# Kernel tuning notes

Measured on AMD Instinct MI355X. Metric: run time of the kernel, lower is better.

The kernel has to match this reference:

```python
import jax, jax.numpy as jnp
import numpy as np

N = 50000
E = 800000
IN_DIM = 128
HIDDEN = 96
HEADS = 4
HEAD_DIM = HIDDEN // HEADS
NUM_LAYERS = 3
NEG_SLOPE = 0.2


def _gat_layer(h, W, a_l, a_r, b, src, dst):
    # h: [N, F_in], W: [F_in, H*D], a_l/a_r: [H, D], b: [H, D]
    feat = (h @ W).reshape(N, HEADS, HEAD_DIM)          # [N, H, D]
    el = jnp.sum(feat * a_l, axis=-1)                    # [N, H]
    er = jnp.sum(feat * a_r, axis=-1)                    # [N, H]
    e = el[src] + er[dst]                                # [E, H]
    e = jnp.where(e > 0, e, NEG_SLOPE * e)               # leaky_relu
    # edge softmax over incoming edges of each dst node
    m = jax.ops.segment_max(e, dst, num_segments=N)      # [N, H]
    ex = jnp.exp(e - m[dst])                             # [E, H]
    denom = jax.ops.segment_sum(ex, dst, num_segments=N) # [N, H]
    alpha = ex / denom[dst]                              # [E, H]
    msg = feat[src] * alpha[:, :, None]                  # [E, H, D]
    out = jax.ops.segment_sum(msg, dst, num_segments=N)  # [N, H, D]
    out = out + b                                        # bias
    out = jax.nn.elu(out)                                # activation
    return out.reshape(N, HEADS * HEAD_DIM)              # flatten(1)


def setup_inputs() -> dict:
    key = jax.random.key(0)
    ks = jax.random.split(key, 16)
    feats = jax.random.normal(ks[0], (N, IN_DIM), dtype=jnp.float32)
    src = jax.random.randint(ks[1], (E,), 0, N)
    dst = jax.random.randint(ks[2], (E,), 0, N)
    inp = {"feats": feats, "src": src, "dst": dst}
    fin = IN_DIM
    for l in range(NUM_LAYERS):
        s = 1.0 / np.sqrt(fin)
        inp[f"W{l}"] = jax.random.normal(ks[3 + 4 * l], (fin, HIDDEN), dtype=jnp.float32) * s
        inp[f"al{l}"] = jax.random.normal(ks[4 + 4 * l], (HEADS, HEAD_DIM), dtype=jnp.float32) * 0.1
        inp[f"ar{l}"] = jax.random.normal(ks[5 + 4 * l], (HEADS, HEAD_DIM), dtype=jnp.float32) * 0.1
        inp[f"b{l}"] = jnp.zeros((HEADS, HEAD_DIM), dtype=jnp.float32)
        fin = HIDDEN
    return inp


def reference(feats, src, dst, W0, al0, ar0, b0, W1, al1, ar1, b1, W2, al2, ar2, b2):
    h = feats
    params = [(W0, al0, ar0, b0), (W1, al1, ar1, b1), (W2, al2, ar2, b2)]
    for (W, al, ar, b) in params:
        h = _gat_layer(h, W, al, ar, b, src, dst)
    # AvgPooling over all nodes (single graph) -> [1, HIDDEN]
    return jnp.mean(h, axis=0, keepdims=True)
```

## Files before the change

### kernel.cpp

```cpp
#include <hip/hip_runtime.h>
#include <hip/hip_bf16.h>

#define N_NODES 50000
#define E_EDGES 800000
#define IN_DIM  128
#define HIDDEN  96
#define HEADS   4
#define HEAD_DIM 24
#define NEG_SLOPE 0.2f
#define POOL_BLOCKS 256


__global__ void k_hist(const int* __restrict__ dst, int* __restrict__ deg) {
    int e = blockIdx.x * 256 + threadIdx.x;
    if (e < E_EDGES) atomicAdd(&deg[dst[e]], 1);
}

__global__ __launch_bounds__(256) void k_scan1(const int* __restrict__ deg,
                                               int* __restrict__ bsum, int n) {
    int i = blockIdx.x * 256 + threadIdx.x;
    int v = (i < n) ? deg[i] : 0;
#pragma unroll
    for (int s = 1; s < 64; s <<= 1) v += __shfl_xor(v, s);
    __shared__ int ws[4];
    if ((threadIdx.x & 63) == 0) ws[threadIdx.x >> 6] = v;
    __syncthreads();
    if (threadIdx.x == 0) bsum[blockIdx.x] = ws[0] + ws[1] + ws[2] + ws[3];
}

__global__ __launch_bounds__(256) void k_scan3(const int* __restrict__ deg,
                                               const int* __restrict__ bsum,
                                               int* __restrict__ off, int n) {
    int tid = threadIdx.x;
    int lane = tid & 63, wv = tid >> 6;

    int pv = (tid < blockIdx.x) ? bsum[tid] : 0;
#pragma unroll
    for (int s = 1; s < 64; s <<= 1) pv += __shfl_xor(pv, s);

    int i = blockIdx.x * 256 + tid;
    int v = (i < n) ? deg[i] : 0;
    int x = v;
#pragma unroll
    for (int s = 1; s < 64; s <<= 1) {
        int t = __shfl_up(x, s);
        if (lane >= s) x += t;
    }

    __shared__ int wsum[4], wsum2[4];
    if (lane == 63) wsum[wv] = x;
    if (lane == 0)  wsum2[wv] = pv;
    __syncthreads();
    int add = wsum2[0] + wsum2[1] + wsum2[2] + wsum2[3];
    for (int w = 0; w < wv; ++w) add += wsum[w];
    if (i < n) off[i] = x - v + add;
    if (i == n - 1) off[n] = x + add;
}

__global__ void k_fill(const int* __restrict__ src, const int* __restrict__ dst,
                       const int* __restrict__ off, int* __restrict__ cursor,
                       int* __restrict__ ssrc) {
    int e = blockIdx.x * 256 + threadIdx.x;
    if (e < E_EDGES) {
        int d = dst[e];
        int p = off[d] + atomicAdd(&cursor[d], 1);
        ssrc[p] = src[e];
    }
}


template <int K>
__global__ __launch_bounds__(384) void k_gemm(const float* __restrict__ h,
                                              const float* __restrict__ W,
                                              const float* __restrict__ al_g,
                                              const float* __restrict__ ar_g,
                                              float* __restrict__ feat,
                                              float* __restrict__ el,
                                              float* __restrict__ er, int n) {
    constexpr int HL = 64 * K;
    constexpr int PT = 384 * 17;
    constexpr int SM = (HL > PT) ? HL : PT;
    __shared__ float smem[SM];
    float* hl = smem;

    int node0 = blockIdx.x * 64;
    int total4 = 64 * K / 4;
    for (int idx = threadIdx.x; idx < total4; idx += 384) {
        int node = idx / (K / 4);
        int koff = (idx % (K / 4)) * 4;
        float4 v = make_float4(0.f, 0.f, 0.f, 0.f);
        if (node0 + node < n)
            v = *(const float4*)(&h[(size_t)(node0 + node) * K + koff]);
        *(float4*)(&hl[node * K + koff]) = v;
    }
    __syncthreads();
    int grp = threadIdx.x / 48;
    int c = (threadIdx.x % 48) * 2;
    int nb = grp * 8;
    float acc[8][2];
#pragma unroll
    for (int i = 0; i < 8; ++i) acc[i][0] = acc[i][1] = 0.f;
    for (int k = 0; k < K; k += 4) {
        float2 w0 = *(const float2*)&W[(k + 0) * 96 + c];
        float2 w1 = *(const float2*)&W[(k + 1) * 96 + c];
        float2 w2 = *(const float2*)&W[(k + 2) * 96 + c];
        float2 w3 = *(const float2*)&W[(k + 3) * 96 + c];
#pragma unroll
        for (int i = 0; i < 8; ++i) {
            float4 hv = *(const float4*)&hl[(nb + i) * K + k];
            acc[i][0] = fmaf(hv.x, w0.x, acc[i][0]);
            acc[i][1] = fmaf(hv.x, w0.y, acc[i][1]);
            acc[i][0] = fmaf(hv.y, w1.x, acc[i][0]);
            acc[i][1] = fmaf(hv.y, w1.y, acc[i][1]);
            acc[i][0] = fmaf(hv.z, w2.x, acc[i][0]);
            acc[i][1] = fmaf(hv.z, w2.y, acc[i][1]);
            acc[i][0] = fmaf(hv.w, w3.x, acc[i][0]);
            acc[i][1] = fmaf(hv.w, w3.y, acc[i][1]);
        }
    }
#pragma unroll
    for (int i = 0; i < 8; ++i) {
        int node = node0 + nb + i;
        if (node < n) *(float2*)&feat[(size_t)node * 96 + c] = make_float2(acc[i][0], acc[i][1]);
    }
    float alc0 = al_g[c], alc1 = al_g[c + 1];
    float arc0 = ar_g[c], arc1 = ar_g[c + 1];
    __syncthreads();
    float* part = smem;
    int base = threadIdx.x * 17;
#pragma unroll
    for (int i = 0; i < 8; ++i) {
        part[base + i * 2]     = acc[i][0] * alc0 + acc[i][1] * alc1;
        part[base + i * 2 + 1] = acc[i][0] * arc0 + acc[i][1] * arc1;
    }
    __syncthreads();
    if (threadIdx.x < 256) {
        int ig = threadIdx.x >> 2;
        int hh = threadIdx.x & 3;
        int g2 = ig >> 3, il = ig & 7;
        float se = 0.f, sr = 0.f;
#pragma unroll
        for (int cc = 0; cc < 12; ++cc) {
            int t = g2 * 48 + hh * 12 + cc;
            se += part[t * 17 + il * 2];
            sr += part[t * 17 + il * 2 + 1];
        }
        int node = node0 + ig;
        if (node < n) {
            el[node * 4 + hh] = se;
            er[node * 4 + hh] = sr;
        }
    }
}

__global__ __launch_bounds__(256) void k_agg(const int* __restrict__ off,
                                             const int* __restrict__ ssrc,
                                             const float* __restrict__ el,
                                             const float* __restrict__ er,
                                             const float* __restrict__ feat,
                                             const float* __restrict__ bias,
                                             float* __restrict__ out) {
    int n = blockIdx.x * 4 + (threadIdx.x >> 6);
    if (n >= N_NODES) return;
    int lane = threadIdx.x & 63;
    int j0   = lane >> 3;
    int h    = (lane >> 1) & 3;
    int half = lane & 1;
    int cbase = h * 24 + half * 12;
    unsigned cboff = (unsigned)cbase * 4u;

    int start = off[n], deg = off[n + 1] - start;
    float er_h = er[(unsigned)n * 4u + h];

    float e_reg[4];
    unsigned s_reg[4];
    float lmax = -1e30f;
#pragma unroll
    for (int t = 0; t < 4; ++t) {
        int j = t * 8 + j0;
        bool act = (j < deg);
        unsigned s = act ? (unsigned)ssrc[start + j] : 0u;
        float e = -1e30f;
        if (act) {
            e = el[s * 4u + h] + er_h;
            e = (e > 0.f) ? e : NEG_SLOPE * e;
        }
        s_reg[t] = s;
        e_reg[t] = e;
        lmax = fmaxf(lmax, e);
    }
    for (int j = 32 + j0; j < deg; j += 8) {
        unsigned s = (unsigned)ssrc[start + j];
        float e = el[s * 4u + h] + er_h;
        e = (e > 0.f) ? e : NEG_SLOPE * e;
        lmax = fmaxf(lmax, e);
    }
    lmax = fmaxf(lmax, __shfl_xor(lmax, 8));
    lmax = fmaxf(lmax, __shfl_xor(lmax, 16));
    lmax = fmaxf(lmax, __shfl_xor(lmax, 32));
    float m = lmax;

    float acc[12];
#pragma unroll
    for (int c = 0; c < 12; ++c) acc[c] = 0.f;
    float den = 0.f;
#pragma unroll
    for (int t = 0; t < 4; ++t) {
        int j = t * 8 + j0;
        if (j < deg) {
            float ex = __expf(e_reg[t] - m);
            den += ex;
            const float* fr = (const float*)((const char*)feat + (size_t)(s_reg[t] * 384u + cboff));
            float4 v0 = *(const float4*)(fr + 0);
            float4 v1 = *(const float4*)(fr + 4);
            float4 v2 = *(const float4*)(fr + 8);
            acc[0] = fmaf(ex, v0.x, acc[0]);  acc[1] = fmaf(ex, v0.y, acc[1]);
            acc[2] = fmaf(ex, v0.z, acc[2]);  acc[3] = fmaf(ex, v0.w, acc[3]);
            acc[4] = fmaf(ex, v1.x, acc[4]);  acc[5] = fmaf(ex, v1.y, acc[5]);
            acc[6] = fmaf(ex, v1.z, acc[6]);  acc[7] = fmaf(ex, v1.w, acc[7]);
            acc[8] = fmaf(ex, v2.x, acc[8]);  acc[9] = fmaf(ex, v2.y, acc[9]);
            acc[10] = fmaf(ex, v2.z, acc[10]); acc[11] = fmaf(ex, v2.w, acc[11]);
        }
    }
    for (int j = 32 + j0; j < deg; j += 8) {
        unsigned s = (unsigned)ssrc[start + j];
        float e = el[s * 4u + h] + er_h;
        e = (e > 0.f) ? e : NEG_SLOPE * e;
        float ex = __expf(e - m);
        den += ex;
        const float* fr = (const float*)((const char*)feat + (size_t)(s * 384u + cboff));
        float4 v0 = *(const float4*)(fr + 0);
        float4 v1 = *(const float4*)(fr + 4);
        float4 v2 = *(const float4*)(fr + 8);
        acc[0] = fmaf(ex, v0.x, acc[0]);  acc[1] = fmaf(ex, v0.y, acc[1]);
        acc[2] = fmaf(ex, v0.z, acc[2]);  acc[3] = fmaf(ex, v0.w, acc[3]);
        acc[4] = fmaf(ex, v1.x, acc[4]);  acc[5] = fmaf(ex, v1.y, acc[5]);
        acc[6] = fmaf(ex, v1.z, acc[6]);  acc[7] = fmaf(ex, v1.w, acc[7]);
        acc[8] = fmaf(ex, v2.x, acc[8]);  acc[9] = fmaf(ex, v2.y, acc[9]);
        acc[10] = fmaf(ex, v2.z, acc[10]); acc[11] = fmaf(ex, v2.w, acc[11]);
    }

#pragma unroll
    for (int st = 8; st <= 32; st <<= 1) {
        den += __shfl_xor(den, st);
#pragma unroll
        for (int c = 0; c < 12; ++c) acc[c] += __shfl_xor(acc[c], st);
    }

    if (j0 == 0) {
        float rden = (den > 0.f) ? 1.f / den : 0.f;
        const float* bp = &bias[cbase];
        float o[12];
#pragma unroll
        for (int c = 0; c < 12; ++c) {
            float v = acc[c] * rden + bp[c];
            o[c] = (v > 0.f) ? v : (__expf(v) - 1.f);
        }
        float* op = &out[(size_t)n * 96 + cbase];
        *(float4*)(op + 0) = make_float4(o[0], o[1], o[2], o[3]);
        *(float4*)(op + 4) = make_float4(o[4], o[5], o[6], o[7]);
        *(float4*)(op + 8) = make_float4(o[8], o[9], o[10], o[11]);
    }
}

__global__ __launch_bounds__(384) void k_pool1(const float* __restrict__ h,
                                               float* __restrict__ partial) {
    int r = threadIdx.x / 96;
    int c = threadIdx.x % 96;
    float a = 0.f;
    for (int nrow = blockIdx.x * 4 + r; nrow < N_NODES; nrow += POOL_BLOCKS * 4)
        a += h[(size_t)nrow * 96 + c];
    __shared__ float sred[4][96];
    sred[r][c] = a;
    __syncthreads();
    if (r == 0)
        partial[blockIdx.x * 96 + c] = sred[0][c] + sred[1][c] + sred[2][c] + sred[3][c];
}

__global__ __launch_bounds__(384) void k_pool2(const float* __restrict__ partial,
                                               float* __restrict__ out) {
    int g = threadIdx.x / 96;
    int c = threadIdx.x % 96;
    float a = 0.f;
    for (int b = g; b < POOL_BLOCKS; b += 4)
        a += partial[b * 96 + c];
    __shared__ float sred[4][96];
    sred[g][c] = a;
    __syncthreads();
    if (g == 0)
        out[c] = (sred[0][c] + sred[1][c] + sred[2][c] + sred[3][c]) * (1.0f / N_NODES);
}


extern "C" void kernel_launch(void* const* d_in, const int* in_sizes, int n_in,
                              void* d_out, int out_size, void* d_ws, size_t ws_size,
                              hipStream_t stream) {
    const float* feats = (const float*)d_in[0];
    const int* src = (const int*)d_in[1];
    const int* dst = (const int*)d_in[2];

    char* p = (char*)d_ws;
    auto alloc = [&](size_t bytes) {
        void* r = (void*)p;
        p += (bytes + 255) & ~(size_t)255;
        return r;
    };
    float* A       = (float*)alloc((size_t)N_NODES * 96 * 4);
    float* B       = (float*)alloc((size_t)N_NODES * 96 * 4);
    float* el      = (float*)alloc((size_t)N_NODES * 4 * 4);
    float* er      = (float*)alloc((size_t)N_NODES * 4 * 4);
    int* degcur    = (int*)alloc((size_t)N_NODES * 2 * 4);
    int* off       = (int*)alloc((size_t)(N_NODES + 1) * 4);
    int* bsum      = (int*)alloc((size_t)256 * 4);
    int* ssrc      = (int*)alloc((size_t)E_EDGES * 4);
    float* partial = (float*)alloc((size_t)POOL_BLOCKS * 96 * 4);
    int* deg = degcur;
    int* cursor = degcur + N_NODES;

    hipMemsetAsync(degcur, 0, (size_t)N_NODES * 2 * 4, stream);

    const int NB = (N_NODES + 255) / 256;
    k_hist<<<(E_EDGES + 255) / 256, 256, 0, stream>>>(dst, deg);
    k_scan1<<<NB, 256, 0, stream>>>(deg, bsum, N_NODES);
    k_scan3<<<NB, 256, 0, stream>>>(deg, bsum, off, N_NODES);
    k_fill<<<(E_EDGES + 255) / 256, 256, 0, stream>>>(src, dst, off, cursor, ssrc);

    const float* hin = feats;
    for (int l = 0; l < 3; ++l) {
        const float* W  = (const float*)d_in[3 + 4 * l];
        const float* al = (const float*)d_in[4 + 4 * l];
        const float* ar = (const float*)d_in[5 + 4 * l];
        const float* bb = (const float*)d_in[6 + 4 * l];

        if (l == 0)
            k_gemm<IN_DIM><<<(N_NODES + 63) / 64, 384, 0, stream>>>(hin, W, al, ar, B, el, er, N_NODES);
        else
            k_gemm<HIDDEN><<<(N_NODES + 63) / 64, 384, 0, stream>>>(hin, W, al, ar, B, el, er, N_NODES);

        k_agg<<<(N_NODES + 3) / 4, 256, 0, stream>>>(off, ssrc, el, er, B, bb, A);
        hin = A;
    }

    k_pool1<<<POOL_BLOCKS, 384, 0, stream>>>(A, partial);
    k_pool2<<<1, 384, 0, stream>>>(partial, (float*)d_out);
}
```

Before: 439.5 us.

## Fuse all GAT stages into one persistent cooperative kernel with grid syncs

Replaces the sequence of separate kernel launches (histogram, scans, fill, three GEMM/aggregate pairs, pooling) with one cooperative persistent kernel that loops over work with grid-stride tiles and uses grid.sync between phases. Layer-0 GEMM now runs before the CSR build inside the same launch. The aim is to remove launch overhead and the memset. The cost is that blocks are limited to the occupancy-resident count, and the aggregate phase uses 384-thread blocks with a large static shared array, which may lower occupancy. Each grid-wide barrier also adds latency.

```diff
diff --git a/kernel.cpp b/kernel.cpp
--- a/kernel.cpp
+++ b/kernel.cpp
@@ -1,303 +1,347 @@
 #include <hip/hip_runtime.h>
-#include <hip/hip_bf16.h>
+#include <hip/hip_cooperative_groups.h>
+
+namespace cg = cooperative_groups;
 
 #define N_NODES 50000
 #define E_EDGES 800000
 #define IN_DIM  128
 #define HIDDEN  96
-#define HEADS   4
-#define HEAD_DIM 24
 #define NEG_SLOPE 0.2f
-#define POOL_BLOCKS 256
-
-
-__global__ void k_hist(const int* __restrict__ dst, int* __restrict__ deg) {
-    int e = blockIdx.x * 256 + threadIdx.x;
-    if (e < E_EDGES) atomicAdd(&deg[dst[e]], 1);
-}
-
-__global__ __launch_bounds__(256) void k_scan1(const int* __restrict__ deg,
-                                               int* __restrict__ bsum, int n) {
-    int i = blockIdx.x * 256 + threadIdx.x;
-    int v = (i < n) ? deg[i] : 0;
-#pragma unroll
-    for (int s = 1; s < 64; s <<= 1) v += __shfl_xor(v, s);
-    __shared__ int ws[4];
-    if ((threadIdx.x & 63) == 0) ws[threadIdx.x >> 6] = v;
-    __syncthreads();
-    if (threadIdx.x == 0) bsum[blockIdx.x] = ws[0] + ws[1] + ws[2] + ws[3];
-}
-
-__global__ __launch_bounds__(256) void k_scan3(const int* __restrict__ deg,
-                                               const int* __restrict__ bsum,
-                                               int* __restrict__ off, int n) {
-    int tid = threadIdx.x;
-    int lane = tid & 63, wv = tid >> 6;
-
-    int pv = (tid < blockIdx.x) ? bsum[tid] : 0;
-#pragma unroll
-    for (int s = 1; s < 64; s <<= 1) pv += __shfl_xor(pv, s);
-
-    int i = blockIdx.x * 256 + tid;
-    int v = (i < n) ? deg[i] : 0;
-    int x = v;
-#pragma unroll
-    for (int s = 1; s < 64; s <<= 1) {
-        int t = __shfl_up(x, s);
-        if (lane >= s) x += t;
-    }
-
-    __shared__ int wsum[4], wsum2[4];
-    if (lane == 63) wsum[wv] = x;
-    if (lane == 0)  wsum2[wv] = pv;
-    __syncthreads();
-    int add = wsum2[0] + wsum2[1] + wsum2[2] + wsum2[3];
-    for (int w = 0; w < wv; ++w) add += wsum[w];
-    if (i < n) off[i] = x - v + add;
-    if (i == n - 1) off[n] = x + add;
-}
-
-__global__ void k_fill(const int* __restrict__ src, const int* __restrict__ dst,
-                       const int* __restrict__ off, int* __restrict__ cursor,
-                       int* __restrict__ ssrc) {
-    int e = blockIdx.x * 256 + threadIdx.x;
-    if (e < E_EDGES) {
-        int d = dst[e];
-        int p = off[d] + atomicAdd(&cursor[d], 1);
-        ssrc[p] = src[e];
-    }
-}
-
+#define NCH ((N_NODES + 255) / 256)
+
+struct Params {
+    const float* feats; const int* src; const int* dst;
+    const float* W[3]; const float* al[3]; const float* ar[3]; const float* bb[3];
+    float* A; float* B; float* el; float* er;
+    int* degcur; int* off; int* bsum; int* ssrc;
+    float* partial; float* out; int nblk;
+};
 
 template <int K>
-__global__ __launch_bounds__(384) void k_gemm(const float* __restrict__ h,
-                                              const float* __restrict__ W,
-                                              const float* __restrict__ al_g,
-                                              const float* __restrict__ ar_g,
-                                              float* __restrict__ feat,
-                                              float* __restrict__ el,
-                                              float* __restrict__ er, int n) {
-    constexpr int HL = 64 * K;
-    constexpr int PT = 384 * 17;
-    constexpr int SM = (HL > PT) ? HL : PT;
-    __shared__ float smem[SM];
-    float* hl = smem;
-
-    int node0 = blockIdx.x * 64;
-    int total4 = 64 * K / 4;
-    for (int idx = threadIdx.x; idx < total4; idx += 384) {
-        int node = idx / (K / 4);
-        int koff = (idx % (K / 4)) * 4;
-        float4 v = make_float4(0.f, 0.f, 0.f, 0.f);
-        if (node0 + node < n)
-            v = *(const float4*)(&h[(size_t)(node0 + node) * K + koff]);
-        *(float4*)(&hl[node * K + koff]) = v;
-    }
-    __syncthreads();
-    int grp = threadIdx.x / 48;
-    int c = (threadIdx.x % 48) * 2;
-    int nb = grp * 8;
-    float acc[8][2];
-#pragma unroll
-    for (int i = 0; i < 8; ++i) acc[i][0] = acc[i][1] = 0.f;
-    for (int k = 0; k < K; k += 4) {
-        float2 w0 = *(const float2*)&W[(k + 0) * 96 + c];
-        float2 w1 = *(const float2*)&W[(k + 1) * 96 + c];
-        float2 w2 = *(const float2*)&W[(k + 2) * 96 + c];
-        float2 w3 = *(const float2*)&W[(k + 3) * 96 + c];
+__device__ __forceinline__ void gemm_phase(const float* __restrict__ h,
+                                           const float* __restrict__ W,
+                                           const float* __restrict__ al_g,
+                                           const float* __restrict__ ar_g,
+                                           float* __restrict__ feat,
+                                           float* __restrict__ el,
+                                           float* __restrict__ er,
+                                           float* smem, int bid, int nblk) {
+    const int tid = threadIdx.x;
+    for (int t = bid; t * 64 < N_NODES; t += nblk) {
+        int node0 = t * 64;
+        int total4 = 64 * K / 4;
+        for (int idx = tid; idx < total4; idx += 384) {
+            int node = idx / (K / 4);
+            int koff = (idx % (K / 4)) * 4;
+            float4 v = make_float4(0.f, 0.f, 0.f, 0.f);
+            if (node0 + node < N_NODES)
+                v = *(const float4*)(&h[(size_t)(node0 + node) * K + koff]);
+            *(float4*)(&smem[node * K + koff]) = v;
+        }
+        __syncthreads();
+        int grp = tid / 48;
+        int c = (tid % 48) * 2;
+        int nb = grp * 8;
+        float acc[8][2];
+#pragma unroll
+        for (int i = 0; i < 8; ++i) acc[i][0] = acc[i][1] = 0.f;
+        for (int k = 0; k < K; k += 4) {
+            float2 w0 = *(const float2*)&W[(k + 0) * 96 + c];
+            float2 w1 = *(const float2*)&W[(k + 1) * 96 + c];
+            float2 w2 = *(const float2*)&W[(k + 2) * 96 + c];
+            float2 w3 = *(const float2*)&W[(k + 3) * 96 + c];
+#pragma unroll
+            for (int i = 0; i < 8; ++i) {
+                float4 hv = *(const float4*)&smem[(nb + i) * K + k];
+                acc[i][0] = fmaf(hv.x, w0.x, acc[i][0]);
+                acc[i][1] = fmaf(hv.x, w0.y, acc[i][1]);
+                acc[i][0] = fmaf(hv.y, w1.x, acc[i][0]);
+                acc[i][1] = fmaf(hv.y, w1.y, acc[i][1]);
+                acc[i][0] = fmaf(hv.z, w2.x, acc[i][0]);
+                acc[i][1] = fmaf(hv.z, w2.y, acc[i][1]);
+                acc[i][0] = fmaf(hv.w, w3.x, acc[i][0]);
+                acc[i][1] = fmaf(hv.w, w3.y, acc[i][1]);
+            }
+        }
 #pragma unroll
         for (int i = 0; i < 8; ++i) {
-            float4 hv = *(const float4*)&hl[(nb + i) * K + k];
-            acc[i][0] = fmaf(hv.x, w0.x, acc[i][0]);
-            acc[i][1] = fmaf(hv.x, w0.y, acc[i][1]);
-            acc[i][0] = fmaf(hv.y, w1.x, acc[i][0]);
-            acc[i][1] = fmaf(hv.y, w1.y, acc[i][1]);
-            acc[i][0] = fmaf(hv.z, w2.x, acc[i][0]);
-            acc[i][1] = fmaf(hv.z, w2.y, acc[i][1]);
-            acc[i][0] = fmaf(hv.w, w3.x, acc[i][0]);
-            acc[i][1] = fmaf(hv.w, w3.y, acc[i][1]);
-        }
-    }
-#pragma unroll
-    for (int i = 0; i < 8; ++i) {
-        int node = node0 + nb + i;
-        if (node < n) *(float2*)&feat[(size_t)node * 96 + c] = make_float2(acc[i][0], acc[i][1]);
-    }
-    float alc0 = al_g[c], alc1 = al_g[c + 1];
-    float arc0 = ar_g[c], arc1 = ar_g[c + 1];
-    __syncthreads();
-    float* part = smem;
-    int base = threadIdx.x * 17;
-#pragma unroll
-    for (int i = 0; i < 8; ++i) {
-        part[base + i * 2]     = acc[i][0] * alc0 + acc[i][1] * alc1;
-        part[base + i * 2 + 1] = acc[i][0] * arc0 + acc[i][1] * arc1;
-    }
-    __syncthreads();
-    if (threadIdx.x < 256) {
-        int ig = threadIdx.x >> 2;
-        int hh = threadIdx.x & 3;
-        int g2 = ig >> 3, il = ig & 7;
-        float se = 0.f, sr = 0.f;
-#pragma unroll
-        for (int cc = 0; cc < 12; ++cc) {
-            int t = g2 * 48 + hh * 12 + cc;
-            se += part[t * 17 + il * 2];
-            sr += part[t * 17 + il * 2 + 1];
-        }
-        int node = node0 + ig;
-        if (node < n) {
-            el[node * 4 + hh] = se;
-            er[node * 4 + hh] = sr;
-        }
-    }
-}
-
-__global__ __launch_bounds__(256) void k_agg(const int* __restrict__ off,
-                                             const int* __restrict__ ssrc,
-                                             const float* __restrict__ el,
-                                             const float* __restrict__ er,
-                                             const float* __restrict__ feat,
-                                             const float* __restrict__ bias,
-                                             float* __restrict__ out) {
-    int n = blockIdx.x * 4 + (threadIdx.x >> 6);
-    if (n >= N_NODES) return;
-    int lane = threadIdx.x & 63;
-    int j0   = lane >> 3;
-    int h    = (lane >> 1) & 3;
-    int half = lane & 1;
-    int cbase = h * 24 + half * 12;
-    unsigned cboff = (unsigned)cbase * 4u;
-
-    int start = off[n], deg = off[n + 1] - start;
-    float er_h = er[(unsigned)n * 4u + h];
-
-    float e_reg[4];
-    unsigned s_reg[4];
-    float lmax = -1e30f;
-#pragma unroll
-    for (int t = 0; t < 4; ++t) {
-        int j = t * 8 + j0;
-        bool act = (j < deg);
-        unsigned s = act ? (unsigned)ssrc[start + j] : 0u;
-        float e = -1e30f;
-        if (act) {
-            e = el[s * 4u + h] + er_h;
-            e = (e > 0.f) ? e : NEG_SLOPE * e;
-        }
-        s_reg[t] = s;
-        e_reg[t] = e;
-        lmax = fmaxf(lmax, e);
-    }
-    for (int j = 32 + j0; j < deg; j += 8) {
-        unsigned s = (unsigned)ssrc[start + j];
-        float e = el[s * 4u + h] + er_h;
-        e = (e > 0.f) ? e : NEG_SLOPE * e;
-        lmax = fmaxf(lmax, e);
-    }
-    lmax = fmaxf(lmax, __shfl_xor(lmax, 8));
-    lmax = fmaxf(lmax, __shfl_xor(lmax, 16));
-    lmax = fmaxf(lmax, __shfl_xor(lmax, 32));
-    float m = lmax;
-
-    float acc[12];
-#pragma unroll
-    for (int c = 0; c < 12; ++c) acc[c] = 0.f;
-    float den = 0.f;
-#pragma unroll
-    for (int t = 0; t < 4; ++t) {
-        int j = t * 8 + j0;
-        if (j < deg) {
-            float ex = __expf(e_reg[t] - m);
-            den += ex;
-            const float* fr = (const float*)((const char*)feat + (size_t)(s_reg[t] * 384u + cboff));
-            float4 v0 = *(const float4*)(fr + 0);
-            float4 v1 = *(const float4*)(fr + 4);
-            float4 v2 = *(const float4*)(fr + 8);
-            acc[0] = fmaf(ex, v0.x, acc[0]);  acc[1] = fmaf(ex, v0.y, acc[1]);
-            acc[2] = fmaf(ex, v0.z, acc[2]);  acc[3] = fmaf(ex, v0.w, acc[3]);
-            acc[4] = fmaf(ex, v1.x, acc[4]);  acc[5] = fmaf(ex, v1.y, acc[5]);
-            acc[6] = fmaf(ex, v1.z, acc[6]);  acc[7] = fmaf(ex, v1.w, acc[7]);
-            acc[8] = fmaf(ex, v2.x, acc[8]);  acc[9] = fmaf(ex, v2.y, acc[9]);
-            acc[10] = fmaf(ex, v2.z, acc[10]); acc[11] = fmaf(ex, v2.w, acc[11]);
-        }
-    }
-    for (int j = 32 + j0; j < deg; j += 8) {
-        unsigned s = (unsigned)ssrc[start + j];
-        float e = el[s * 4u + h] + er_h;
-        e = (e > 0.f) ? e : NEG_SLOPE * e;
-        float ex = __expf(e - m);
-        den += ex;
-        const float* fr = (const float*)((const char*)feat + (size_t)(s * 384u + cboff));
-        float4 v0 = *(const float4*)(fr + 0);
-        float4 v1 = *(const float4*)(fr + 4);
-        float4 v2 = *(const float4*)(fr + 8);
-        acc[0] = fmaf(ex, v0.x, acc[0]);  acc[1] = fmaf(ex, v0.y, acc[1]);
-        acc[2] = fmaf(ex, v0.z, acc[2]);  acc[3] = fmaf(ex, v0.w, acc[3]);
-        acc[4] = fmaf(ex, v1.x, acc[4]);  acc[5] = fmaf(ex, v1.y, acc[5]);
-        acc[6] = fmaf(ex, v1.z, acc[6]);  acc[7] = fmaf(ex, v1.w, acc[7]);
-        acc[8] = fmaf(ex, v2.x, acc[8]);  acc[9] = fmaf(ex, v2.y, acc[9]);
-        acc[10] = fmaf(ex, v2.z, acc[10]); acc[11] = fmaf(ex, v2.w, acc[11]);
-    }
-
-#pragma unroll
-    for (int st = 8; st <= 32; st <<= 1) {
-        den += __shfl_xor(den, st);
-#pragma unroll
-        for (int c = 0; c < 12; ++c) acc[c] += __shfl_xor(acc[c], st);
-    }
-
-    if (j0 == 0) {
-        float rden = (den > 0.f) ? 1.f / den : 0.f;
-        const float* bp = &bias[cbase];
-        float o[12];
-#pragma unroll
-        for (int c = 0; c < 12; ++c) {
-            float v = acc[c] * rden + bp[c];
-            o[c] = (v > 0.f) ? v : (__expf(v) - 1.f);
-        }
-        float* op = &out[(size_t)n * 96 + cbase];
-        *(float4*)(op + 0) = make_float4(o[0], o[1], o[2], o[3]);
-        *(float4*)(op + 4) = make_float4(o[4], o[5], o[6], o[7]);
-        *(float4*)(op + 8) = make_float4(o[8], o[9], o[10], o[11]);
-    }
-}
-
-__global__ __launch_bounds__(384) void k_pool1(const float* __restrict__ h,
-                                               float* __restrict__ partial) {
-    int r = threadIdx.x / 96;
-    int c = threadIdx.x % 96;
-    float a = 0.f;
-    for (int nrow = blockIdx.x * 4 + r; nrow < N_NODES; nrow += POOL_BLOCKS * 4)
-        a += h[(size_t)nrow * 96 + c];
-    __shared__ float sred[4][96];
-    sred[r][c] = a;
-    __syncthreads();
-    if (r == 0)
-        partial[blockIdx.x * 96 + c] = sred[0][c] + sred[1][c] + sred[2][c] + sred[3][c];
-}
-
-__global__ __launch_bounds__(384) void k_pool2(const float* __restrict__ partial,
-                                               float* __restrict__ out) {
-    int g = threadIdx.x / 96;
-    int c = threadIdx.x % 96;
-    float a = 0.f;
-    for (int b = g; b < POOL_BLOCKS; b += 4)
-        a += partial[b * 96 + c];
-    __shared__ float sred[4][96];
-    sred[g][c] = a;
-    __syncthreads();
-    if (g == 0)
-        out[c] = (sred[0][c] + sred[1][c] + sred[2][c] + sred[3][c]) * (1.0f / N_NODES);
+            int node = node0 + nb + i;
+            if (node < N_NODES)
+                *(float2*)&feat[(size_t)node * 96 + c] = make_float2(acc[i][0], acc[i][1]);
+        }
+        float alc0 = al_g[c], alc1 = al_g[c + 1];
+        float arc0 = ar_g[c], arc1 = ar_g[c + 1];
+        __syncthreads();
+        int base = tid * 17;
+#pragma unroll
+        for (int i = 0; i < 8; ++i) {
+            smem[base + i * 2]     = acc[i][0] * alc0 + acc[i][1] * alc1;
+            smem[base + i * 2 + 1] = acc[i][0] * arc0 + acc[i][1] * arc1;
+        }
+        __syncthreads();
+        if (tid < 256) {
+            int ig = tid >> 2;
+            int hh = tid & 3;
+            int g2 = ig >> 3, il = ig & 7;
+            float se = 0.f, sr = 0.f;
+#pragma unroll
+            for (int cc = 0; cc < 12; ++cc) {
+                int tt = g2 * 48 + hh * 12 + cc;
+                se += smem[tt * 17 + il * 2];
+                sr += smem[tt * 17 + il * 2 + 1];
+            }
+            int node = node0 + ig;
+            if (node < N_NODES) {
+                el[node * 4 + hh] = se;
+                er[node * 4 + hh] = sr;
+            }
+        }
+        __syncthreads();
+    }
+}
+
+__device__ __forceinline__ void agg_phase(const int* __restrict__ off,
+                                          const int* __restrict__ ssrc,
+                                          const float* __restrict__ el,
+                                          const float* __restrict__ er,
+                                          const float* __restrict__ feat,
+                                          const float* __restrict__ bias,
+                                          float* __restrict__ out, int bid, int nblk) {
+    const int tid = threadIdx.x;
+    const int lane = tid & 63;
+    const int wv = tid >> 6;
+    const int j0 = lane >> 3;
+    const int h = (lane >> 1) & 3;
+    const int half = lane & 1;
+    const int cbase = h * 24 + half * 12;
+    const unsigned cboff = (unsigned)cbase * 4u;
+
+    for (int base = bid * 6; base < N_NODES; base += nblk * 6) {
+        int n = base + wv;
+        if (n < N_NODES) {
+            int start = off[n], deg = off[n + 1] - start;
+            float er_h = er[(unsigned)n * 4u + h];
+
+            float e_reg[4];
+            unsigned s_reg[4];
+            float lmax = -1e30f;
+#pragma unroll
+            for (int t = 0; t < 4; ++t) {
+                int j = t * 8 + j0;
+                bool act = (j < deg);
+                unsigned s = act ? (unsigned)ssrc[start + j] : 0u;
+                float e = -1e30f;
+                if (act) {
+                    e = el[s * 4u + h] + er_h;
+                    e = (e > 0.f) ? e : NEG_SLOPE * e;
+                }
+                s_reg[t] = s;
+                e_reg[t] = e;
+                lmax = fmaxf(lmax, e);
+            }
+            for (int j = 32 + j0; j < deg; j += 8) {
+                unsigned s = (unsigned)ssrc[start + j];
+                float e = el[s * 4u + h] + er_h;
+                e = (e > 0.f) ? e : NEG_SLOPE * e;
+                lmax = fmaxf(lmax, e);
+            }
+            lmax = fmaxf(lmax, __shfl_xor(lmax, 8));
+            lmax = fmaxf(lmax, __shfl_xor(lmax, 16));
+            lmax = fmaxf(lmax, __shfl_xor(lmax, 32));
+            float m = lmax;
+
+            float acc[12];
+#pragma unroll
+            for (int c = 0; c < 12; ++c) acc[c] = 0.f;
+            float den = 0.f;
+#pragma unroll
+            for (int t = 0; t < 4; ++t) {
+                int j = t * 8 + j0;
+                if (j < deg) {
+                    float ex = __expf(e_reg[t] - m);
+                    den += ex;
+                    const float* fr = (const float*)((const char*)feat + (size_t)(s_reg[t] * 384u + cboff));
+                    float4 v0 = *(const float4*)(fr + 0);
+                    float4 v1 = *(const float4*)(fr + 4);
+                    float4 v2 = *(const float4*)(fr + 8);
+                    acc[0] = fmaf(ex, v0.x, acc[0]);   acc[1] = fmaf(ex, v0.y, acc[1]);
+                    acc[2] = fmaf(ex, v0.z, acc[2]);   acc[3] = fmaf(ex, v0.w, acc[3]);
+                    acc[4] = fmaf(ex, v1.x, acc[4]);   acc[5] = fmaf(ex, v1.y, acc[5]);
+                    acc[6] = fmaf(ex, v1.z, acc[6]);   acc[7] = fmaf(ex, v1.w, acc[7]);
+                    acc[8] = fmaf(ex, v2.x, acc[8]);   acc[9] = fmaf(ex, v2.y, acc[9]);
+                    acc[10] = fmaf(ex, v2.z, acc[10]); acc[11] = fmaf(ex, v2.w, acc[11]);
+                }
+            }
+            for (int j = 32 + j0; j < deg; j += 8) {
+                unsigned s = (unsigned)ssrc[start + j];
+                float e = el[s * 4u + h] + er_h;
+                e = (e > 0.f) ? e : NEG_SLOPE * e;
+                float ex = __expf(e - m);
+                den += ex;
+                const float* fr = (const float*)((const char*)feat + (size_t)(s * 384u + cboff));
+                float4 v0 = *(const float4*)(fr + 0);
+                float4 v1 = *(const float4*)(fr + 4);
+                float4 v2 = *(const float4*)(fr + 8);
+                acc[0] = fmaf(ex, v0.x, acc[0]);   acc[1] = fmaf(ex, v0.y, acc[1]);
+                acc[2] = fmaf(ex, v0.z, acc[2]);   acc[3] = fmaf(ex, v0.w, acc[3]);
+                acc[4] = fmaf(ex, v1.x, acc[4]);   acc[5] = fmaf(ex, v1.y, acc[5]);
+                acc[6] = fmaf(ex, v1.z, acc[6]);   acc[7] = fmaf(ex, v1.w, acc[7]);
+                acc[8] = fmaf(ex, v2.x, acc[8]);   acc[9] = fmaf(ex, v2.y, acc[9]);
+                acc[10] = fmaf(ex, v2.z, acc[10]); acc[11] = fmaf(ex, v2.w, acc[11]);
+            }
+
+#pragma unroll
+            for (int st = 8; st <= 32; st <<= 1) {
+                den += __shfl_xor(den, st);
+#pragma unroll
+                for (int c = 0; c < 12; ++c) acc[c] += __shfl_xor(acc[c], st);
+            }
+
+            if (j0 == 0) {
+                float rden = (den > 0.f) ? 1.f / den : 0.f;
+                const float* bp = &bias[cbase];
+                float o[12];
+#pragma unroll
+                for (int c = 0; c < 12; ++c) {
+                    float v = acc[c] * rden + bp[c];
+                    o[c] = (v > 0.f) ? v : (__expf(v) - 1.f);
+                }
+                float* op = &out[(size_t)n * 96 + cbase];
+                *(float4*)(op + 0) = make_float4(o[0], o[1], o[2], o[3]);
+                *(float4*)(op + 4) = make_float4(o[4], o[5], o[6], o[7]);
+                *(float4*)(op + 8) = make_float4(o[8], o[9], o[10], o[11]);
+            }
+        }
+    }
+}
+
+__device__ __forceinline__ void scan1_phase(const int* deg, int* bsum, int* ismem,
+                                            int bid, int nblk) {
+    const int tid = threadIdx.x;
+    for (int b = bid; b < NCH; b += nblk) {
+        int i = b * 256 + tid;
+        int v = (tid < 256 && i < N_NODES) ? deg[i] : 0;
+#pragma unroll
+        for (int s = 1; s < 64; s <<= 1) v += __shfl_xor(v, s);
+        if ((tid & 63) == 0) ismem[tid >> 6] = v;
+        __syncthreads();
+        if (tid == 0)
+            bsum[b] = ismem[0] + ismem[1] + ismem[2] + ismem[3] + ismem[4] + ismem[5];
+        __syncthreads();
+    }
+}
+
+__device__ __forceinline__ void scan3_phase(const int* deg, const int* bsum,
+                                            int* off, int* ismem, int bid, int nblk) {
+    const int tid = threadIdx.x;
+    const int lane = tid & 63, wv = tid >> 6;
+    for (int b = bid; b < NCH; b += nblk) {
+        int pv = (tid < b) ? bsum[tid] : 0;
+#pragma unroll
+        for (int s = 1; s < 64; s <<= 1) pv += __shfl_xor(pv, s);
+        int i = b * 256 + tid;
+        int v = (tid < 256 && i < N_NODES) ? deg[i] : 0;
+        int x = v;
+#pragma unroll
+        for (int s = 1; s < 64; s <<= 1) {
+            int t2 = __shfl_up(x, s);
+            if (lane >= s) x += t2;
+        }
+        if (lane == 63) ismem[wv] = x;
+        if (lane == 0)  ismem[8 + wv] = pv;
+        __syncthreads();
+        int add = ismem[8] + ismem[9] + ismem[10] + ismem[11] + ismem[12] + ismem[13];
+        for (int w = 0; w < wv; ++w) add += ismem[w];
+        if (tid < 256 && i < N_NODES) off[i] = x - v + add;
+        if (i == N_NODES - 1) off[N_NODES] = x + add;
+        __syncthreads();
+    }
+}
+
+__global__ __launch_bounds__(384) void mega(Params P) {
+    __shared__ float smem[8192];
+    int* ismem = (int*)smem;
+    cg::grid_group grid = cg::this_grid();
+    const int bid = blockIdx.x;
+    const int nblk = P.nblk;
+    const int tid = threadIdx.x;
+
+    for (int i = bid * 384 + tid; i < N_NODES * 2; i += nblk * 384) P.degcur[i] = 0;
+    gemm_phase<IN_DIM>(P.feats, P.W[0], P.al[0], P.ar[0], P.B, P.el, P.er, smem, bid, nblk);
+    grid.sync();
+
+    for (int e = bid * 384 + tid; e < E_EDGES; e += nblk * 384)
+        atomicAdd(&P.degcur[P.dst[e]], 1);
+    grid.sync();
+
+    scan1_phase(P.degcur, P.bsum, ismem, bid, nblk);
+    grid.sync();
+
+    scan3_phase(P.degcur, P.bsum, P.off, ismem, bid, nblk);
+    grid.sync();
+
+    {
+        int* cursor = P.degcur + N_NODES;
+        for (int e = bid * 384 + tid; e < E_EDGES; e += nblk * 384) {
+            int d = P.dst[e];
+            int p = P.off[d] + atomicAdd(&cursor[d], 1);
+            P.ssrc[p] = P.src[e];
+        }
+    }
+    grid.sync();
+
+    agg_phase(P.off, P.ssrc, P.el, P.er, P.B, P.bb[0], P.A, bid, nblk);
+    grid.sync();
+    gemm_phase<HIDDEN>(P.A, P.W[1], P.al[1], P.ar[1], P.B, P.el, P.er, smem, bid, nblk);
+    grid.sync();
+    agg_phase(P.off, P.ssrc, P.el, P.er, P.B, P.bb[1], P.A, bid, nblk);
+    grid.sync();
+    gemm_phase<HIDDEN>(P.A, P.W[2], P.al[2], P.ar[2], P.B, P.el, P.er, smem, bid, nblk);
+    grid.sync();
+    agg_phase(P.off, P.ssrc, P.el, P.er, P.B, P.bb[2], P.A, bid, nblk);
+    grid.sync();
+
+    {
+        int r = tid / 96, c = tid % 96;
+        float a = 0.f;
+        for (int nr = bid * 4 + r; nr < N_NODES; nr += nblk * 4)
+            a += P.A[(size_t)nr * 96 + c];
+        __syncthreads();
+        smem[tid] = a;
+        __syncthreads();
+        if (tid < 96)
+            P.partial[bid * 96 + tid] =
+                smem[tid] + smem[96 + tid] + smem[192 + tid] + smem[288 + tid];
+    }
+    grid.sync();
+
+    if (bid == 0) {
+        int g = tid / 96, c = tid % 96;
+        float a = 0.f;
+        for (int b = g; b < nblk; b += 4) a += P.partial[b * 96 + c];
+        smem[tid] = a;
+        __syncthreads();
+        if (tid < 96)
+            P.out[tid] = (smem[tid] + smem[96 + tid] + smem[192 + tid] + smem[288 + tid]) *
+                         (1.0f / N_NODES);
+    }
 }
 
 
 extern "C" void kernel_launch(void* const* d_in, const int* in_sizes, int n_in,
                               void* d_out, int out_size, void* d_ws, size_t ws_size,
                               hipStream_t stream) {
-    const float* feats = (const float*)d_in[0];
-    const int* src = (const int*)d_in[1];
-    const int* dst = (const int*)d_in[2];
+    Params pr;
+    pr.feats = (const float*)d_in[0];
+    pr.src   = (const int*)d_in[1];
+    pr.dst   = (const int*)d_in[2];
+    for (int l = 0; l < 3; ++l) {
+        pr.W[l]  = (const float*)d_in[3 + 4 * l];
+        pr.al[l] = (const float*)d_in[4 + 4 * l];
+        pr.ar[l] = (const float*)d_in[5 + 4 * l];
+        pr.bb[l] = (const float*)d_in[6 + 4 * l];
+    }
 
     char* p = (char*)d_ws;
     auto alloc = [&](size_t bytes) {
@@ -305,42 +349,29 @@
         p += (bytes + 255) & ~(size_t)255;
         return r;
     };
-    float* A       = (float*)alloc((size_t)N_NODES * 96 * 4);
-    float* B       = (float*)alloc((size_t)N_NODES * 96 * 4);
-    float* el      = (float*)alloc((size_t)N_NODES * 4 * 4);
-    float* er      = (float*)alloc((size_t)N_NODES * 4 * 4);
-    int* degcur    = (int*)alloc((size_t)N_NODES * 2 * 4);
-    int* off       = (int*)alloc((size_t)(N_NODES + 1) * 4);
-    int* bsum      = (int*)alloc((size_t)256 * 4);
-    int* ssrc      = (int*)alloc((size_t)E_EDGES * 4);
-    float* partial = (float*)alloc((size_t)POOL_BLOCKS * 96 * 4);
-    int* deg = degcur;
-    int* cursor = degcur + N_NODES;
-
-    hipMemsetAsync(degcur, 0, (size_t)N_NODES * 2 * 4, stream);
-
-    const int NB = (N_NODES + 255) / 256;
-    k_hist<<<(E_EDGES + 255) / 256, 256, 0, stream>>>(dst, deg);
-    k_scan1<<<NB, 256, 0, stream>>>(deg, bsum, N_NODES);
-    k_scan3<<<NB, 256, 0, stream>>>(deg, bsum, off, N_NODES);
-    k_fill<<<(E_EDGES + 255) / 256, 256, 0, stream>>>(src, dst, off, cursor, ssrc);
-
-    const float* hin = feats;
-    for (int l = 0; l < 3; ++l) {
-        const float* W  = (const float*)d_in[3 + 4 * l];
-        const float* al = (const float*)d_in[4 + 4 * l];
-        const float* ar = (const float*)d_in[5 + 4 * l];
-        const float* bb = (const float*)d_in[6 + 4 * l];
-
-        if (l == 0)
-            k_gemm<IN_DIM><<<(N_NODES + 63) / 64, 384, 0, stream>>>(hin, W, al, ar, B, el, er, N_NODES);
-        else
-            k_gemm<HIDDEN><<<(N_NODES + 63) / 64, 384, 0, stream>>>(hin, W, al, ar, B, el, er, N_NODES);
-
-        k_agg<<<(N_NODES + 3) / 4, 256, 0, stream>>>(off, ssrc, el, er, B, bb, A);
-        hin = A;
-    }
-
-    k_pool1<<<POOL_BLOCKS, 384, 0, stream>>>(A, partial);
-    k_pool2<<<1, 384, 0, stream>>>(partial, (float*)d_out);
-}
+    pr.A       = (float*)alloc((size_t)N_NODES * 96 * 4);
+    pr.B       = (float*)alloc((size_t)N_NODES * 96 * 4);
+    pr.el      = (float*)alloc((size_t)N_NODES * 4 * 4);
+    pr.er      = (float*)alloc((size_t)N_NODES * 4 * 4);
+    pr.degcur  = (int*)alloc((size_t)N_NODES * 2 * 4);
+    pr.off     = (int*)alloc((size_t)(N_NODES + 1) * 4);
+    pr.bsum    = (int*)alloc((size_t)NCH * 4);
+    pr.ssrc    = (int*)alloc((size_t)E_EDGES * 4);
+    pr.partial = (float*)alloc((size_t)2048 * 96 * 4);
+    pr.out     = (float*)d_out;
+
+    int dev = 0;
+    hipGetDevice(&dev);
+    int nSM = 0;
+    hipDeviceGetAttribute(&nSM, hipDeviceAttributeMultiprocessorCount, dev);
+    if (nSM <= 0) nSM = 256;
+    int maxB = 0;
+    hipOccupancyMaxActiveBlocksPerMultiprocessor(&maxB, mega, 384, 0);
+    if (maxB < 1) maxB = 1;
+    int nblk = nSM * maxB;
+    if (nblk > 2048) nblk = 2048;
+    pr.nblk = nblk;
+
+    void* args[] = { &pr };
+    hipLaunchCooperativeKernel((void*)mega, dim3(nblk), dim3(384), args, 0, stream);
+}
```

Result: slower. 988.2 us (+124.8%).
